# Performance work log

Hardware: AMD Instinct MI355X
Metric: run time of the kernel (lower is better)

The kernel has to match this reference:

```python
import jax, jax.numpy as jnp
import numpy as np

D_MODEL = 1024
NUM_HEADS = 16
HEAD_DIM = D_MODEL // NUM_HEADS


def setup_inputs() -> dict:
    key = jax.random.key(0)
    ks = jax.random.split(key, 11)
    B, S, D = 4, 2048, D_MODEL
    s = 1.0 / np.sqrt(D)
    inp = {
        "query": jax.random.normal(ks[0], (B, S, D), jnp.float32),
        "key": jax.random.normal(ks[1], (B, S, D), jnp.float32),
        "value": jax.random.normal(ks[2], (B, S, D), jnp.float32),
        # linear params (torch nn.Linear: y = x @ W.T + b); store as [in, out]
        "Wq": jax.random.uniform(ks[3], (D, D), jnp.float32, -s, s),
        "bq": jax.random.uniform(ks[4], (D,), jnp.float32, -s, s),
        "Wk": jax.random.uniform(ks[5], (D, D), jnp.float32, -s, s),
        "bk": jax.random.uniform(ks[6], (D,), jnp.float32, -s, s),
        "Wv": jax.random.uniform(ks[7], (D, D), jnp.float32, -s, s),
        "bv": jax.random.uniform(ks[8], (D,), jnp.float32, -s, s),
        "Wo": jax.random.uniform(ks[9], (D, D), jnp.float32, -s, s),
        "bo": jax.random.uniform(ks[10], (D,), jnp.float32, -s, s),
    }
    return inp


def _split_heads(x):
    B, S, D = x.shape
    return x.reshape(B, S, NUM_HEADS, HEAD_DIM).transpose(0, 2, 1, 3)  # [B,H,S,d]


def reference(query, key, value, Wq, bq, Wk, bk, Wv, bv, Wo, bo):
    q = _split_heads(query @ Wq + bq)
    k = _split_heads(key @ Wk + bk)
    v = _split_heads(value @ Wv + bv)
    scores = jnp.einsum("bhqd,bhkd->bhqk", q, k) / np.sqrt(HEAD_DIM).astype(np.float32)
    attn = jax.nn.softmax(scores, axis=-1)
    # dropout is identity in eval/deterministic mode
    ctx = jnp.einsum("bhqk,bhkd->bhqd", attn, v)
    B, H, S, d = ctx.shape
    ctx = ctx.transpose(0, 2, 1, 3).reshape(B, S, H * d)
    out = ctx @ Wo + bo
    return out, attn
```

## Files before the change

### kernel.cpp

```cpp
#include <hip/hip_runtime.h>
#include <hip/hip_bf16.h>
#include <math.h>

#define S_LEN  2048
#define BATCH  4
#define NHEAD  16
#define HDIM   64
#define DMODEL 1024
#define NTOK   (BATCH * S_LEN)
#define BHEADS (BATCH * NHEAD)

typedef __attribute__((ext_vector_type(8))) short bfrag;
typedef __attribute__((ext_vector_type(4))) float f32x4;
typedef __attribute__((ext_vector_type(4))) ushort u16x4;

__device__ inline ushort f2bf(float f) {
  union { float f; unsigned u; } v; v.f = f;
  unsigned r = (v.u + 0x7FFFu + ((v.u >> 16) & 1u)) >> 16;
  return (ushort)r;
}

__device__ inline ushort bfh(float f) {
  union { float f; unsigned u; } v; v.f = f;
  return (ushort)((v.u + 0x8000u) >> 16);
}

__device__ inline void gload_lds16(const void* g, void* lds) {
  __builtin_amdgcn_global_load_lds(
      (const __attribute__((address_space(1))) unsigned int*)g,
      (__attribute__((address_space(3))) unsigned int*)lds, 16, 0, 0);
}

__global__ __launch_bounds__(256) void convert_qkv(
    const float* xq, const float* xk, const float* xv,
    ushort* oq, ushort* ok, ushort* ov) {
  const float* src = (blockIdx.y == 0) ? xq : (blockIdx.y == 1) ? xk : xv;
  ushort* dst      = (blockIdx.y == 0) ? oq : (blockIdx.y == 1) ? ok : ov;
  const int n4 = NTOK * DMODEL / 4;
  for (int i = blockIdx.x * blockDim.x + threadIdx.x; i < n4;
       i += gridDim.x * blockDim.x) {
    float4 f = reinterpret_cast<const float4*>(src)[i];
    ushort4 o;
    o.x = f2bf(f.x); o.y = f2bf(f.y); o.z = f2bf(f.z); o.w = f2bf(f.w);
    reinterpret_cast<ushort4*>(dst)[i] = o;
  }
}

__global__ __launch_bounds__(256) void wtrans(const float* w, ushort* wt) {
  __shared__ float t[64][65];
  const int k0 = (blockIdx.x >> 4) * 64;
  const int n0 = (blockIdx.x & 15) * 64;
  for (int i = threadIdx.x; i < 4096; i += 256) {
    int r = i >> 6, c = i & 63;
    t[r][c] = w[(size_t)(k0 + r) * DMODEL + n0 + c];
  }
  __syncthreads();
  for (int i = threadIdx.x; i < 4096; i += 256) {
    int r = i >> 6, c = i & 63;
    wt[(size_t)(n0 + r) * DMODEL + k0 + c] = f2bf(t[c][r]);
  }
}

__global__ __launch_bounds__(256) void vtrans(const ushort* v, ushort* vt) {
  __shared__ ushort t[64][65];
  const int bh = blockIdx.y;
  const int s0 = blockIdx.x * 64;
  const ushort* vb = v  + (size_t)bh * S_LEN * HDIM;
  ushort*       vo = vt + (size_t)bh * HDIM * S_LEN;
  for (int i = threadIdx.x; i < 4096; i += 256) {
    int r = i >> 6, c = i & 63;
    t[r][c] = vb[(size_t)(s0 + r) * HDIM + c];
  }
  __syncthreads();
  for (int i = threadIdx.x; i < 4096; i += 256) {
    int r = i >> 6, c = i & 63;
    vo[(size_t)r * S_LEN + s0 + c] = t[c][r];
  }
}

template <int MODE>
__global__ __launch_bounds__(256) void gemm_bt(
    const ushort* A0, const ushort* A1, const ushort* A2,
    const ushort* B0, const ushort* B1, const ushort* B2,
    const float* c0, const float* c1, const float* c2,
    void* o0, void* o1, void* o2, int M, int N, int K) {
  const int z = blockIdx.z;
  const ushort* A  = z == 0 ? A0 : z == 1 ? A1 : A2;
  const ushort* Bt = z == 0 ? B0 : z == 1 ? B1 : B2;
  const float* bias = z == 0 ? c0 : z == 1 ? c1 : c2;
  void* dst = z == 0 ? o0 : z == 1 ? o1 : o2;

  __shared__ __align__(16) ushort As[128][32];
  __shared__ __align__(16) ushort Bs[128][32];
  const int tid  = threadIdx.x;
  const int wid  = tid >> 6;
  const int l15  = tid & 15;
  const int lh   = (tid & 63) >> 4;
  const int row0 = blockIdx.x * 128;
  const int col0 = blockIdx.y * 128;
  const int wr   = (wid >> 1) * 64;
  const int wc   = (wid & 1) * 64;

  f32x4 acc[4][4] = {};

  for (int kt = 0; kt < K; kt += 32) {
#pragma unroll
    for (int j = 0; j < 2; ++j) {
      const int toff = (j * 256 + tid) * 16;
      const int r    = toff >> 6;
      const int cb   = toff & 63;
      gload_lds16(A + (size_t)(row0 + r) * K + kt + (cb >> 1),
                  (char*)(&As[0][0]) + (j * 256 + wid * 64) * 16);
      gload_lds16(Bt + (size_t)(col0 + r) * K + kt + (cb >> 1),
                  (char*)(&Bs[0][0]) + (j * 256 + wid * 64) * 16);
    }
    __syncthreads();
    bfrag av[4], bv[4];
#pragma unroll
    for (int m = 0; m < 4; ++m) av[m] = *(const bfrag*)&As[wr + m * 16 + l15][lh * 8];
#pragma unroll
    for (int n = 0; n < 4; ++n) bv[n] = *(const bfrag*)&Bs[wc + n * 16 + l15][lh * 8];
#pragma unroll
    for (int m = 0; m < 4; ++m)
#pragma unroll
      for (int n = 0; n < 4; ++n)
        acc[m][n] = __builtin_amdgcn_mfma_f32_16x16x32_bf16(av[m], bv[n], acc[m][n], 0, 0, 0);
    __syncthreads();
  }

#pragma unroll
  for (int m = 0; m < 4; ++m) {
#pragma unroll
    for (int n = 0; n < 4; ++n) {
#pragma unroll
      for (int r = 0; r < 4; ++r) {
        const int grow = row0 + wr + m * 16 + lh * 4 + r;
        const int gcol = col0 + wc + n * 16 + l15;
        const float v = acc[m][n][r] + bias[gcol];
        if (MODE == 0) {
          ((float*)dst)[(size_t)grow * N + gcol] = v;
        } else {
          const size_t o = (((size_t)(grow >> 11) * NHEAD + (gcol >> 6)) * S_LEN +
                            (grow & 2047)) * HDIM + (gcol & 63);
          ((ushort*)dst)[o] = f2bf(v);
        }
      }
    }
  }
}

__global__ __launch_bounds__(256) void attn_kernel(
    const ushort* Q, const ushort* K, const ushort* Vt, float* attn, ushort* ctx) {
  const int b0    = blockIdx.x;
  const int xcd   = b0 & 7;
  const int inner = b0 >> 3;
  const int bh    = xcd + ((inner >> 5) << 3);
  const int qt    = inner & 31;
  const int b  = bh >> 4;
  const int h  = bh & 15;
  const int q0 = qt * 64;
  const int wid  = threadIdx.x >> 6;
  const int lane = threadIdx.x & 63;
  const int l15  = lane & 15;
  const int lh   = lane >> 4;

  const ushort* Qb = Q  + ((size_t)bh * S_LEN + q0 + wid * 16) * HDIM;
  const ushort* Kb = K  + (size_t)bh * S_LEN * HDIM;
  const ushort* Vb = Vt + (size_t)bh * HDIM * S_LEN;

  __shared__ __align__(16) ushort Ks[2][32 * 64];
  __shared__ __align__(16) ushort Vs[2][64 * 32];
  __shared__ __align__(16) ushort Plds[4][16][40];

  const int tK     = threadIdx.x;
  const int krow   = tK >> 3;
  const int kchk_s = (tK & 7) ^ (krow & 7);
  const int vrow   = tK >> 2;
  const int vchk_s = (tK & 3) ^ (vrow & 3);

  const int ksw0 = ((lh ^ (l15 & 7)) * 8);
  const int ksw1 = (((lh + 4) ^ (l15 & 7)) * 8);
  const int vsw  = ((lh ^ (l15 & 3)) * 8);

  const bfrag qf0 = *(const bfrag*)&Qb[(size_t)l15 * HDIM + lh * 8];
  const bfrag qf1 = *(const bfrag*)&Qb[(size_t)l15 * HDIM + 32 + lh * 8];

  const float c = 0.125f * 1.44269504089f;
  const int NT = S_LEN / 32;

  gload_lds16(Kb + (size_t)krow * HDIM + kchk_s * 8, (char*)&Ks[0][0] + wid * 1024);
  int cur = 0;
  float lr = 0.f;
  for (int t = 0; t < NT; ++t) {
    __syncthreads();
    if (t + 1 < NT)
      gload_lds16(Kb + (size_t)((t + 1) * 32 + krow) * HDIM + kchk_s * 8,
                  (char*)&Ks[cur ^ 1][0] + wid * 1024);
    const bfrag ca0 = *(const bfrag*)&Ks[cur][l15 * 64 + ksw0];
    const bfrag ca1 = *(const bfrag*)&Ks[cur][l15 * 64 + ksw1];
    const bfrag cb0 = *(const bfrag*)&Ks[cur][(16 + l15) * 64 + ksw0];
    const bfrag cb1 = *(const bfrag*)&Ks[cur][(16 + l15) * 64 + ksw1];
    f32x4 sa = {}, sb = {};
    __builtin_amdgcn_s_setprio(1);
    sa = __builtin_amdgcn_mfma_f32_16x16x32_bf16(ca0, qf0, sa, 0, 0, 0);
    sa = __builtin_amdgcn_mfma_f32_16x16x32_bf16(ca1, qf1, sa, 0, 0, 0);
    sb = __builtin_amdgcn_mfma_f32_16x16x32_bf16(cb0, qf0, sb, 0, 0, 0);
    sb = __builtin_amdgcn_mfma_f32_16x16x32_bf16(cb1, qf1, sb, 0, 0, 0);
    __builtin_amdgcn_s_setprio(0);
#pragma unroll
    for (int r = 0; r < 4; ++r)
      lr += exp2f(sa[r] * c) + exp2f(sb[r] * c);
    cur ^= 1;
  }
  lr += __shfl_xor(lr, 16);
  lr += __shfl_xor(lr, 32);
  const float linv = __builtin_amdgcn_rcpf(lr);

  f32x4 cacc[4] = {};
  float* arow = attn + ((size_t)bh * S_LEN + q0 + wid * 16 + l15) * S_LEN;

  gload_lds16(Kb + (size_t)krow * HDIM + kchk_s * 8, (char*)&Ks[0][0] + wid * 1024);
  gload_lds16(Vb + (size_t)vrow * S_LEN + vchk_s * 8, (char*)&Vs[0][0] + wid * 1024);
  __builtin_amdgcn_sched_barrier(0);
  asm volatile("s_waitcnt vmcnt(0)" ::: "memory");
  __builtin_amdgcn_s_barrier();
  __builtin_amdgcn_sched_barrier(0);
  cur = 0;
  for (int t = 0; t < NT; ++t) {
    const int k0 = t * 32;
    if (t + 1 < NT) {
      gload_lds16(Kb + (size_t)(k0 + 32 + krow) * HDIM + kchk_s * 8,
                  (char*)&Ks[cur ^ 1][0] + wid * 1024);
      gload_lds16(Vb + (size_t)vrow * S_LEN + k0 + 32 + vchk_s * 8,
                  (char*)&Vs[cur ^ 1][0] + wid * 1024);
    }
    const bfrag ca0 = *(const bfrag*)&Ks[cur][l15 * 64 + ksw0];
    const bfrag ca1 = *(const bfrag*)&Ks[cur][l15 * 64 + ksw1];
    const bfrag cb0 = *(const bfrag*)&Ks[cur][(16 + l15) * 64 + ksw0];
    const bfrag cb1 = *(const bfrag*)&Ks[cur][(16 + l15) * 64 + ksw1];
    const bfrag vf0 = *(const bfrag*)&Vs[cur][(0 * 16 + l15) * 32 + vsw];
    const bfrag vf1 = *(const bfrag*)&Vs[cur][(1 * 16 + l15) * 32 + vsw];
    const bfrag vf2 = *(const bfrag*)&Vs[cur][(2 * 16 + l15) * 32 + vsw];
    const bfrag vf3 = *(const bfrag*)&Vs[cur][(3 * 16 + l15) * 32 + vsw];

    f32x4 sa = {}, sb = {};
    __builtin_amdgcn_s_setprio(1);
    sa = __builtin_amdgcn_mfma_f32_16x16x32_bf16(ca0, qf0, sa, 0, 0, 0);
    sa = __builtin_amdgcn_mfma_f32_16x16x32_bf16(ca1, qf1, sa, 0, 0, 0);
    sb = __builtin_amdgcn_mfma_f32_16x16x32_bf16(cb0, qf0, sb, 0, 0, 0);
    sb = __builtin_amdgcn_mfma_f32_16x16x32_bf16(cb1, qf1, sb, 0, 0, 0);
    __builtin_amdgcn_s_setprio(0);

    f32x4 pa, pb;
#pragma unroll
    for (int r = 0; r < 4; ++r) pa[r] = exp2f(sa[r] * c) * linv;
#pragma unroll
    for (int r = 0; r < 4; ++r) pb[r] = exp2f(sb[r] * c) * linv;

    __builtin_nontemporal_store(pa, (f32x4*)(arow + k0 + lh * 4));
    __builtin_nontemporal_store(pb, (f32x4*)(arow + k0 + 16 + lh * 4));

    u16x4 ua = {bfh(pa[0]), bfh(pa[1]), bfh(pa[2]), bfh(pa[3])};
    u16x4 ub = {bfh(pb[0]), bfh(pb[1]), bfh(pb[2]), bfh(pb[3])};
    *(u16x4*)&Plds[wid][l15][lh * 4]      = ua;
    *(u16x4*)&Plds[wid][l15][16 + lh * 4] = ub;

    const bfrag pf = *(const bfrag*)&Plds[wid][l15][lh * 8];
    __builtin_amdgcn_s_setprio(1);
    cacc[0] = __builtin_amdgcn_mfma_f32_16x16x32_bf16(pf, vf0, cacc[0], 0, 0, 0);
    cacc[1] = __builtin_amdgcn_mfma_f32_16x16x32_bf16(pf, vf1, cacc[1], 0, 0, 0);
    cacc[2] = __builtin_amdgcn_mfma_f32_16x16x32_bf16(pf, vf2, cacc[2], 0, 0, 0);
    cacc[3] = __builtin_amdgcn_mfma_f32_16x16x32_bf16(pf, vf3, cacc[3], 0, 0, 0);
    __builtin_amdgcn_s_setprio(0);

    __builtin_amdgcn_sched_barrier(0);
    asm volatile("s_waitcnt vmcnt(2)" ::: "memory");
    __builtin_amdgcn_s_barrier();
    __builtin_amdgcn_sched_barrier(0);
    cur ^= 1;
  }

#pragma unroll
  for (int n = 0; n < 4; ++n) {
#pragma unroll
    for (int r = 0; r < 4; ++r) {
      const size_t tok = (size_t)b * S_LEN + q0 + wid * 16 + lh * 4 + r;
      ctx[tok * DMODEL + h * HDIM + n * 16 + l15] = f2bf(cacc[n][r]);
    }
  }
}

extern "C" void kernel_launch(void* const* d_in, const int* in_sizes, int n_in,
                              void* d_out, int out_size, void* d_ws, size_t ws_size,
                              hipStream_t stream) {
  const float* Xq = (const float*)d_in[0];
  const float* Xk = (const float*)d_in[1];
  const float* Xv = (const float*)d_in[2];
  const float* Wq = (const float*)d_in[3];
  const float* bq = (const float*)d_in[4];
  const float* Wk = (const float*)d_in[5];
  const float* bk = (const float*)d_in[6];
  const float* Wv = (const float*)d_in[7];
  const float* bv = (const float*)d_in[8];
  const float* Wo = (const float*)d_in[9];
  const float* bo = (const float*)d_in[10];

  float* out  = (float*)d_out;
  float* attn = out + (size_t)NTOK * DMODEL;

  char* ws = (char*)d_ws;
  const size_t XB = (size_t)NTOK * DMODEL * 2;
  const size_t WB = (size_t)DMODEL * DMODEL * 2;
  ushort* xq  = (ushort*)(ws);
  ushort* xk  = (ushort*)(ws + XB);
  ushort* xv  = (ushort*)(ws + 2 * XB);
  ushort* wqt = (ushort*)(ws + 3 * XB);
  ushort* wkt = (ushort*)(ws + 3 * XB + WB);
  ushort* wvt = (ushort*)(ws + 3 * XB + 2 * WB);
  ushort* wot = (ushort*)(ws + 3 * XB + 3 * WB);
  ushort* qh  = (ushort*)(ws + 3 * XB + 4 * WB);
  ushort* kh  = (ushort*)(ws + 4 * XB + 4 * WB);
  ushort* vh  = (ushort*)(ws + 5 * XB + 4 * WB);
  ushort* vt  = (ushort*)(ws + 6 * XB + 4 * WB);
  ushort* ctx = (ushort*)(ws + 7 * XB + 4 * WB);

  convert_qkv<<<dim3(1024, 3), 256, 0, stream>>>(Xq, Xk, Xv, xq, xk, xv);
  wtrans<<<256, 256, 0, stream>>>(Wq, wqt);
  wtrans<<<256, 256, 0, stream>>>(Wk, wkt);
  wtrans<<<256, 256, 0, stream>>>(Wv, wvt);
  wtrans<<<256, 256, 0, stream>>>(Wo, wot);

  gemm_bt<1><<<dim3(64, 8, 3), 256, 0, stream>>>(
      xq, xk, xv, wqt, wkt, wvt, bq, bk, bv,
      (void*)qh, (void*)kh, (void*)vh, NTOK, DMODEL, DMODEL);

  vtrans<<<dim3(32, BHEADS), 256, 0, stream>>>(vh, vt);

  attn_kernel<<<dim3(S_LEN / 64 * BHEADS), 256, 0, stream>>>(qh, kh, vt, attn, ctx);

  gemm_bt<0><<<dim3(64, 8, 1), 256, 0, stream>>>(
      ctx, ctx, ctx, wot, wot, wot, bo, bo, bo,
      (void*)out, (void*)out, (void*)out, NTOK, DMODEL, DMODEL);
}
```

Baseline: 544.1 us.

## Split attention into two kernels with triple-buffered K/V prefetch

```diff
diff --git a/kernel.cpp b/kernel.cpp
--- a/kernel.cpp
+++ b/kernel.cpp
@@ -30,6 +30,8 @@
       (const __attribute__((address_space(1))) unsigned int*)g,
       (__attribute__((address_space(3))) unsigned int*)lds, 16, 0, 0);
 }
+
+#define SBAR() __builtin_amdgcn_sched_barrier(0)
 
 __global__ __launch_bounds__(256) void convert_qkv(
     const float* xq, const float* xk, const float* xv,
@@ -149,8 +151,82 @@
   }
 }
 
-__global__ __launch_bounds__(256) void attn_kernel(
-    const ushort* Q, const ushort* K, const ushort* Vt, float* attn, ushort* ctx) {
+__global__ __launch_bounds__(256) void attn_pass1(
+    const ushort* Q, const ushort* K, float* linv_ws) {
+  const int b0    = blockIdx.x;
+  const int xcd   = b0 & 7;
+  const int inner = b0 >> 3;
+  const int bh    = xcd + ((inner >> 5) << 3);
+  const int qt    = inner & 31;
+  const int q0 = qt * 64;
+  const int wid  = threadIdx.x >> 6;
+  const int lane = threadIdx.x & 63;
+  const int l15  = lane & 15;
+  const int lh   = lane >> 4;
+
+  const ushort* Qb = Q + ((size_t)bh * S_LEN + q0 + wid * 16) * HDIM;
+  const ushort* Kb = K + (size_t)bh * S_LEN * HDIM;
+
+  __shared__ __align__(16) ushort Ks[3][32 * 64];
+
+  const int krow   = threadIdx.x >> 3;
+  const int kchk_s = (threadIdx.x & 7) ^ (krow & 7);
+  const int ksw0 = ((lh ^ (l15 & 7)) * 8);
+  const int ksw1 = (((lh + 4) ^ (l15 & 7)) * 8);
+
+  const bfrag qf0 = *(const bfrag*)&Qb[(size_t)l15 * HDIM + lh * 8];
+  const bfrag qf1 = *(const bfrag*)&Qb[(size_t)l15 * HDIM + 32 + lh * 8];
+
+  const float c = 0.125f * 1.44269504089f;
+  const int NT = S_LEN / 32;
+
+  gload_lds16(Kb + (size_t)(0 * 32 + krow) * HDIM + kchk_s * 8, (char*)&Ks[0][0] + wid * 1024);
+  gload_lds16(Kb + (size_t)(1 * 32 + krow) * HDIM + kchk_s * 8, (char*)&Ks[1][0] + wid * 1024);
+  SBAR();
+  asm volatile("s_waitcnt vmcnt(1)" ::: "memory");
+  __builtin_amdgcn_s_barrier();
+  SBAR();
+
+  int cur = 0;
+  float lr = 0.f;
+  for (int t = 0; t < NT; ++t) {
+    if (t + 2 < NT) {
+      int s2 = cur + 2; if (s2 >= 3) s2 -= 3;
+      gload_lds16(Kb + (size_t)((t + 2) * 32 + krow) * HDIM + kchk_s * 8,
+                  (char*)&Ks[s2][0] + wid * 1024);
+    }
+    const bfrag ca0 = *(const bfrag*)&Ks[cur][l15 * 64 + ksw0];
+    const bfrag ca1 = *(const bfrag*)&Ks[cur][l15 * 64 + ksw1];
+    const bfrag cb0 = *(const bfrag*)&Ks[cur][(16 + l15) * 64 + ksw0];
+    const bfrag cb1 = *(const bfrag*)&Ks[cur][(16 + l15) * 64 + ksw1];
+    f32x4 sa = {}, sb = {};
+    __builtin_amdgcn_s_setprio(1);
+    sa = __builtin_amdgcn_mfma_f32_16x16x32_bf16(ca0, qf0, sa, 0, 0, 0);
+    sa = __builtin_amdgcn_mfma_f32_16x16x32_bf16(ca1, qf1, sa, 0, 0, 0);
+    sb = __builtin_amdgcn_mfma_f32_16x16x32_bf16(cb0, qf0, sb, 0, 0, 0);
+    sb = __builtin_amdgcn_mfma_f32_16x16x32_bf16(cb1, qf1, sb, 0, 0, 0);
+    __builtin_amdgcn_s_setprio(0);
+#pragma unroll
+    for (int r = 0; r < 4; ++r)
+      lr += exp2f(sa[r] * c) + exp2f(sb[r] * c);
+    if (t < NT - 1) {
+      SBAR();
+      if (t < NT - 2) asm volatile("s_waitcnt vmcnt(1)" ::: "memory");
+      else            asm volatile("s_waitcnt vmcnt(0)" ::: "memory");
+      __builtin_amdgcn_s_barrier();
+      SBAR();
+    }
+    cur = cur + 1; if (cur >= 3) cur -= 3;
+  }
+  lr += __shfl_xor(lr, 16);
+  lr += __shfl_xor(lr, 32);
+  if (lh == 0)
+    linv_ws[(size_t)bh * S_LEN + q0 + wid * 16 + l15] = __builtin_amdgcn_rcpf(lr);
+}
+
+__global__ __launch_bounds__(256) void attn_pass2(
+    const ushort* Q, const ushort* K, const ushort* Vt, const float* linv_ws,
+    float* attn, ushort* ctx) {
   const int b0    = blockIdx.x;
   const int xcd   = b0 & 7;
   const int inner = b0 >> 3;
@@ -168,15 +244,14 @@
   const ushort* Kb = K  + (size_t)bh * S_LEN * HDIM;
   const ushort* Vb = Vt + (size_t)bh * HDIM * S_LEN;
 
-  __shared__ __align__(16) ushort Ks[2][32 * 64];
-  __shared__ __align__(16) ushort Vs[2][64 * 32];
+  __shared__ __align__(16) ushort Ks[3][32 * 64];
+  __shared__ __align__(16) ushort Vs[3][64 * 32];
   __shared__ __align__(16) ushort Plds[4][16][40];
 
-  const int tK     = threadIdx.x;
-  const int krow   = tK >> 3;
-  const int kchk_s = (tK & 7) ^ (krow & 7);
-  const int vrow   = tK >> 2;
-  const int vchk_s = (tK & 3) ^ (vrow & 3);
+  const int krow   = threadIdx.x >> 3;
+  const int kchk_s = (threadIdx.x & 7) ^ (krow & 7);
+  const int vrow   = threadIdx.x >> 2;
+  const int vchk_s = (threadIdx.x & 3) ^ (vrow & 3);
 
   const int ksw0 = ((lh ^ (l15 & 7)) * 8);
   const int ksw1 = (((lh + 4) ^ (l15 & 7)) * 8);
@@ -184,55 +259,32 @@
 
   const bfrag qf0 = *(const bfrag*)&Qb[(size_t)l15 * HDIM + lh * 8];
   const bfrag qf1 = *(const bfrag*)&Qb[(size_t)l15 * HDIM + 32 + lh * 8];
+  const float linv = linv_ws[(size_t)bh * S_LEN + q0 + wid * 16 + l15];
 
   const float c = 0.125f * 1.44269504089f;
   const int NT = S_LEN / 32;
 
-  gload_lds16(Kb + (size_t)krow * HDIM + kchk_s * 8, (char*)&Ks[0][0] + wid * 1024);
-  int cur = 0;
-  float lr = 0.f;
-  for (int t = 0; t < NT; ++t) {
-    __syncthreads();
-    if (t + 1 < NT)
-      gload_lds16(Kb + (size_t)((t + 1) * 32 + krow) * HDIM + kchk_s * 8,
-                  (char*)&Ks[cur ^ 1][0] + wid * 1024);
-    const bfrag ca0 = *(const bfrag*)&Ks[cur][l15 * 64 + ksw0];
-    const bfrag ca1 = *(const bfrag*)&Ks[cur][l15 * 64 + ksw1];
-    const bfrag cb0 = *(const bfrag*)&Ks[cur][(16 + l15) * 64 + ksw0];
-    const bfrag cb1 = *(const bfrag*)&Ks[cur][(16 + l15) * 64 + ksw1];
-    f32x4 sa = {}, sb = {};
-    __builtin_amdgcn_s_setprio(1);
-    sa = __builtin_amdgcn_mfma_f32_16x16x32_bf16(ca0, qf0, sa, 0, 0, 0);
-    sa = __builtin_amdgcn_mfma_f32_16x16x32_bf16(ca1, qf1, sa, 0, 0, 0);
-    sb = __builtin_amdgcn_mfma_f32_16x16x32_bf16(cb0, qf0, sb, 0, 0, 0);
-    sb = __builtin_amdgcn_mfma_f32_16x16x32_bf16(cb1, qf1, sb, 0, 0, 0);
-    __builtin_amdgcn_s_setprio(0);
-#pragma unroll
-    for (int r = 0; r < 4; ++r)
-      lr += exp2f(sa[r] * c) + exp2f(sb[r] * c);
-    cur ^= 1;
-  }
-  lr += __shfl_xor(lr, 16);
-  lr += __shfl_xor(lr, 32);
-  const float linv = __builtin_amdgcn_rcpf(lr);
-
   f32x4 cacc[4] = {};
   float* arow = attn + ((size_t)bh * S_LEN + q0 + wid * 16 + l15) * S_LEN;
 
-  gload_lds16(Kb + (size_t)krow * HDIM + kchk_s * 8, (char*)&Ks[0][0] + wid * 1024);
-  gload_lds16(Vb + (size_t)vrow * S_LEN + vchk_s * 8, (char*)&Vs[0][0] + wid * 1024);
-  __builtin_amdgcn_sched_barrier(0);
-  asm volatile("s_waitcnt vmcnt(0)" ::: "memory");
+  gload_lds16(Kb + (size_t)(0 * 32 + krow) * HDIM + kchk_s * 8, (char*)&Ks[0][0] + wid * 1024);
+  gload_lds16(Vb + (size_t)vrow * S_LEN + 0  + vchk_s * 8,      (char*)&Vs[0][0] + wid * 1024);
+  gload_lds16(Kb + (size_t)(1 * 32 + krow) * HDIM + kchk_s * 8, (char*)&Ks[1][0] + wid * 1024);
+  gload_lds16(Vb + (size_t)vrow * S_LEN + 32 + vchk_s * 8,      (char*)&Vs[1][0] + wid * 1024);
+  SBAR();
+  asm volatile("s_waitcnt vmcnt(2)" ::: "memory");
   __builtin_amdgcn_s_barrier();
-  __builtin_amdgcn_sched_barrier(0);
-  cur = 0;
+  SBAR();
+
+  int cur = 0;
   for (int t = 0; t < NT; ++t) {
     const int k0 = t * 32;
-    if (t + 1 < NT) {
-      gload_lds16(Kb + (size_t)(k0 + 32 + krow) * HDIM + kchk_s * 8,
-                  (char*)&Ks[cur ^ 1][0] + wid * 1024);
-      gload_lds16(Vb + (size_t)vrow * S_LEN + k0 + 32 + vchk_s * 8,
-                  (char*)&Vs[cur ^ 1][0] + wid * 1024);
+    if (t + 2 < NT) {
+      int s2 = cur + 2; if (s2 >= 3) s2 -= 3;
+      gload_lds16(Kb + (size_t)(k0 + 64 + krow) * HDIM + kchk_s * 8,
+                  (char*)&Ks[s2][0] + wid * 1024);
+      gload_lds16(Vb + (size_t)vrow * S_LEN + k0 + 64 + vchk_s * 8,
+                  (char*)&Vs[s2][0] + wid * 1024);
     }
     const bfrag ca0 = *(const bfrag*)&Ks[cur][l15 * 64 + ksw0];
     const bfrag ca1 = *(const bfrag*)&Ks[cur][l15 * 64 + ksw1];
@@ -273,11 +325,14 @@
     cacc[3] = __builtin_amdgcn_mfma_f32_16x16x32_bf16(pf, vf3, cacc[3], 0, 0, 0);
     __builtin_amdgcn_s_setprio(0);
 
-    __builtin_amdgcn_sched_barrier(0);
-    asm volatile("s_waitcnt vmcnt(2)" ::: "memory");
-    __builtin_amdgcn_s_barrier();
-    __builtin_amdgcn_sched_barrier(0);
-    cur ^= 1;
+    if (t < NT - 1) {
+      SBAR();
+      if (t < NT - 2) asm volatile("s_waitcnt vmcnt(6)" ::: "memory");
+      else            asm volatile("s_waitcnt vmcnt(4)" ::: "memory");
+      __builtin_amdgcn_s_barrier();
+      SBAR();
+    }
+    cur = cur + 1; if (cur >= 3) cur -= 3;
   }
 
 #pragma unroll
@@ -323,6 +378,7 @@
   ushort* vh  = (ushort*)(ws + 5 * XB + 4 * WB);
   ushort* vt  = (ushort*)(ws + 6 * XB + 4 * WB);
   ushort* ctx = (ushort*)(ws + 7 * XB + 4 * WB);
+  float*  liw = (float*)(ws + 8 * XB + 4 * WB);
 
   convert_qkv<<<dim3(1024, 3), 256, 0, stream>>>(Xq, Xk, Xv, xq, xk, xv);
   wtrans<<<256, 256, 0, stream>>>(Wq, wqt);
@@ -336,7 +392,8 @@
 
   vtrans<<<dim3(32, BHEADS), 256, 0, stream>>>(vh, vt);
 
-  attn_kernel<<<dim3(S_LEN / 64 * BHEADS), 256, 0, stream>>>(qh, kh, vt, attn, ctx);
+  attn_pass1<<<dim3(S_LEN / 64 * BHEADS), 256, 0, stream>>>(qh, kh, liw);
+  attn_pass2<<<dim3(S_LEN / 64 * BHEADS), 256, 0, stream>>>(qh, kh, vt, liw, attn, ctx);
 
   gemm_bt<0><<<dim3(64, 8, 1), 256, 0, stream>>>(
       ctx, ctx, ctx, wot, wot, wot, bo, bo, bo,
```

New measurement: 604.6 us. +11.1%, slower.
